# Optimization experiments

Hardware: AMD Instinct MI355X
Metric: run time of the kernel (lower is better)

Reference implementation:

```python
import jax, jax.numpy as jnp
import numpy as np

B, T, DIN, DC, CS = 8, 4096, 1024, 256, 8192
EPS = 1e-12

def _l2norm(x):
    # F.normalize: x / max(||x||_2, eps) along last axis
    n = jnp.sqrt(jnp.sum(x * x, axis=-1, keepdims=True))
    return x / jnp.maximum(n, EPS)

def _wn(v, g):
    # torch weight_norm(dim=0): w = g * v / ||v|| per output row
    n = jnp.sqrt(jnp.sum(v * v, axis=1, keepdims=True))
    return g * v / jnp.maximum(n, EPS)

def setup_inputs() -> dict:
    key = jax.random.key(0)
    k = jax.random.split(key, 4)
    return {
        "z": jax.random.normal(k[0], (B, DIN, T), jnp.float32),
        "in_v": jax.random.normal(k[1], (DC, DIN), jnp.float32) * 0.02,
        "in_g": jnp.ones((DC, 1), jnp.float32),
        "in_b": jnp.zeros((DC,), jnp.float32),
        "out_v": jax.random.normal(k[2], (DIN, DC), jnp.float32) * 0.02,
        "out_g": jnp.ones((DIN, 1), jnp.float32),
        "out_b": jnp.zeros((DIN,), jnp.float32),
        "codebook": jax.random.normal(k[3], (CS, DC), jnp.float32),
    }

def reference(z, in_v, in_g, in_b, out_v, out_g, out_b, codebook):
    b, _, t = z.shape
    w_in = _wn(in_v, in_g)                      # (DC, DIN)
    z_e = jnp.einsum('bdt,cd->bct', z, w_in) + in_b[None, :, None]  # (B, DC, T)

    # decode_latents (eval mode: dropout p=0)
    enc = _l2norm(z_e.transpose(0, 2, 1).reshape(b * t, -1))   # (BT, DC)
    cb = _l2norm(codebook)                                     # (CS, DC)
    dist = (jnp.sum(enc * enc, axis=1, keepdims=True)
            - 2.0 * enc @ cb.T
            + jnp.sum(cb * cb, axis=1)[None, :])               # (BT, CS)
    indices = jnp.argmax(-dist, axis=1).reshape(b, t)          # (B, T)
    z_q = codebook[indices].transpose(0, 2, 1)                 # (B, DC, T)

    commitment_loss = jnp.mean((z_e - jax.lax.stop_gradient(z_q)) ** 2, axis=(1, 2))
    codebook_loss = jnp.mean((z_q - jax.lax.stop_gradient(z_e)) ** 2, axis=(1, 2))

    z_q_st = z_e + jax.lax.stop_gradient(z_q - z_e)            # straight-through
    w_out = _wn(out_v, out_g)                                  # (DIN, DC)
    z_q_out = jnp.einsum('bct,dc->bdt', z_q_st, w_out) + out_b[None, :, None]
    return (z_q_out, commitment_loss, codebook_loss, indices)
```

## Files before the change

### kernel.cpp

```cpp
#include <hip/hip_runtime.h>
#include <stdint.h>

#define BB 8
#define TT 4096
#define DIN 1024
#define DC 256
#define CS 8192
#define EPSF 1e-12f

typedef unsigned short ushort_t;
typedef __attribute__((ext_vector_type(8))) short short8;
typedef __attribute__((ext_vector_type(4))) float f32x4;

constexpr size_t OFF_WIN   = 0;
constexpr size_t OFF_WOUTT = OFF_WIN   + 1048576;
constexpr size_t OFF_CBN   = OFF_WOUTT + 1048576;
constexpr size_t OFF_NRM2  = OFF_CBN   + 8388608;
constexpr size_t OFF_ZE    = OFF_NRM2  + 32768;
constexpr size_t OFF_INV   = OFF_ZE    + 33554432;
constexpr size_t OFF_ENC2  = OFF_INV   + 131072;
constexpr size_t OFF_KEYS  = OFF_ENC2  + 131072;
constexpr size_t OFF_LOSS  = OFF_KEYS  + 262144;
constexpr size_t OFF_WSPL  = OFF_LOSS  + 256;
constexpr size_t OFF_W2T   = OFF_WSPL  + 1048576;
constexpr size_t REQ_WS_ZE = OFF_W2T + 134217728ull;

__device__ __forceinline__ float block_reduce_sum_256(float v, float* sbuf) {
  #pragma unroll
  for (int o = 32; o > 0; o >>= 1) v += __shfl_down(v, o, 64);
  int lane = threadIdx.x & 63, w = threadIdx.x >> 6;
  if (lane == 0) sbuf[w] = v;
  __syncthreads();
  float r = sbuf[0] + sbuf[1] + sbuf[2] + sbuf[3];
  __syncthreads();
  return r;
}

__device__ __forceinline__ ushort_t bf16_rne(float x) {
  unsigned u = __float_as_uint(x);
  unsigned r = (u + 0x7FFFu + ((u >> 16) & 1u)) >> 16;
  return (ushort_t)r;
}
__device__ __forceinline__ float bf16f(ushort_t h) {
  return __uint_as_float(((unsigned)h) << 16);
}

__device__ __forceinline__ int swz4(int r) {
  return (r + (r >> 2)) & 3;
}

__device__ __forceinline__ void async_copy16(const ushort_t* g, ushort_t* lds) {
  __builtin_amdgcn_global_load_lds(
      (const __attribute__((address_space(1))) void*)g,
      (__attribute__((address_space(3))) void*)lds, 16, 0, 0);
}

__device__ __forceinline__ void stage_tile8(const ushort_t* __restrict__ s0,
                                            ushort_t* __restrict__ dstbuf,
                                            const int (&go)[8]) {
  #pragma unroll
  for (int i = 0; i < 8; i++) async_copy16(s0 + go[i], dstbuf + i*512);
}

__device__ __forceinline__ void stage2(const ushort_t* __restrict__ srcbase,
                                       ushort_t* __restrict__ comp,
                                       const int (&go)[2], int wu) {
  async_copy16(srcbase + go[0], comp + wu);
  async_copy16(srcbase + go[1], comp + wu + 4096);
}

#define LD8(base, off) (*(const short8*)((const char*)(base) + (off)))

template<int MH, int CLO>
__device__ __forceinline__ void qmfma(f32x4 (&acc)[8][4],
    const short8 (&fah)[4], const short8 (&fal)[4],
    const short8 (&fbh)[4], const short8 (&fbl)[4]) {
  #pragma unroll
  for (int r = 0; r < 4; r++) {
    #pragma unroll
    for (int c2 = 0; c2 < 2; c2++) {
      f32x4 t = acc[MH*4 + r][CLO + c2];
      t = __builtin_amdgcn_mfma_f32_16x16x32_bf16(fah[r], fbh[CLO + c2], t, 0, 0, 0);
      t = __builtin_amdgcn_mfma_f32_16x16x32_bf16(fal[r], fbh[CLO + c2], t, 0, 0, 0);
      t = __builtin_amdgcn_mfma_f32_16x16x32_bf16(fah[r], fbl[CLO + c2], t, 0, 0, 0);
      acc[MH*4 + r][CLO + c2] = t;
    }
  }
}

__global__ void k_prep_win(const float* __restrict__ v, const float* __restrict__ g,
                           float* __restrict__ w, ushort_t* __restrict__ wh,
                           ushort_t* __restrict__ wl) {
  __shared__ float sb[4];
  int r = blockIdx.x, t = threadIdx.x;
  float xv[4]; float s = 0.f;
  #pragma unroll
  for (int i = 0; i < 4; i++) { xv[i] = v[r*DIN + t + i*256]; s += xv[i]*xv[i]; }
  s = block_reduce_sum_256(s, sb);
  float sc = g[r] / fmaxf(sqrtf(s), EPSF);
  #pragma unroll
  for (int i = 0; i < 4; i++) {
    float val = xv[i] * sc;
    int idx = r*DIN + t + i*256;
    w[idx] = val;
    ushort_t h = bf16_rne(val);
    wh[idx] = h;
    wl[idx] = bf16_rne(val - bf16f(h));
  }
}

__global__ void k_prep_wout(const float* __restrict__ v, const float* __restrict__ g,
                            float* __restrict__ wT) {
  __shared__ float sb[4];
  int r = blockIdx.x, t = threadIdx.x;
  float x = v[r*DC + t];
  float s = block_reduce_sum_256(x*x, sb);
  float sc = g[r] / fmaxf(sqrtf(s), EPSF);
  wT[t*DIN + r] = x * sc;
}

__global__ void k_prep_cb(const float* __restrict__ cb, ushort_t* __restrict__ cbh,
                          ushort_t* __restrict__ cbl, float* __restrict__ nrm2,
                          float* __restrict__ nmraw, float* __restrict__ n2raw) {
  __shared__ float sb[4];
  int j = blockIdx.x, t = threadIdx.x;
  float x = cb[j*DC + t];
  float s = block_reduce_sum_256(x*x, sb);
  float nm = fmaxf(sqrtf(s), EPSF);
  float cn = x / nm;
  ushort_t h = bf16_rne(cn);
  cbh[j*DC + t] = h;
  cbl[j*DC + t] = bf16_rne(cn - bf16f(h));
  float q = block_reduce_sum_256(cn*cn, sb);
  if (t == 0) { nrm2[j] = q; nmraw[j] = nm; n2raw[j] = s; }
}

__global__ void k_split_cbraw(const float* __restrict__ cb, ushort_t* __restrict__ ch,
                              ushort_t* __restrict__ cl) {
  int j = blockIdx.x, t = threadIdx.x;
  float x = cb[j*DC + t];
  ushort_t h = bf16_rne(x);
  ch[j*DC + t] = h;
  cl[j*DC + t] = bf16_rne(x - bf16f(h));
}

__global__ void k_split_wout(const float* __restrict__ v, const float* __restrict__ g,
                             ushort_t* __restrict__ wh, ushort_t* __restrict__ wl) {
  __shared__ float sb[4];
  int r = blockIdx.x, t = threadIdx.x;
  float x = v[r*DC + t];
  float s = block_reduce_sum_256(x*x, sb);
  float sc = g[r] / fmaxf(sqrtf(s), EPSF);
  float val = x * sc;
  ushort_t h = bf16_rne(val);
  wh[r*DC + t] = h;
  wl[r*DC + t] = bf16_rne(val - bf16f(h));
}

template<bool BIAS>
__global__ __launch_bounds__(256) void k_gemm(
    const float* __restrict__ A, const float* __restrict__ Bmat,
    const float* __restrict__ bias, float* __restrict__ C,
    int K, int lda, int ldb, int ldc, size_t strideB, size_t strideC)
{
  __shared__ float As[16][132];
  __shared__ float Bs[16][132];
  const int bn = blockIdx.x * 128;
  const int bm = blockIdx.y * 128;
  const float* Bb = Bmat + (size_t)blockIdx.z * strideB;
  float* Cb = C + (size_t)blockIdx.z * strideC;
  const int tid = threadIdx.x;
  const int tx = tid & 15, ty = tid >> 4;
  const int am = tid & 127, akq = (tid >> 7) * 8;
  const int bk = tid >> 5, bj = (tid & 31) * 4;

  float acc[8][8];
  #pragma unroll
  for (int i = 0; i < 8; i++)
    #pragma unroll
    for (int j = 0; j < 8; j++) acc[i][j] = 0.f;

  for (int k0 = 0; k0 < K; k0 += 16) {
    float4 a0 = *(const float4*)&A[(size_t)(bm+am)*lda + k0 + akq];
    float4 a1 = *(const float4*)&A[(size_t)(bm+am)*lda + k0 + akq + 4];
    float4 b0 = *(const float4*)&Bb[(size_t)(k0+bk)*ldb + bn + bj];
    float4 b1 = *(const float4*)&Bb[(size_t)(k0+bk+8)*ldb + bn + bj];
    As[akq+0][am] = a0.x; As[akq+1][am] = a0.y; As[akq+2][am] = a0.z; As[akq+3][am] = a0.w;
    As[akq+4][am] = a1.x; As[akq+5][am] = a1.y; As[akq+6][am] = a1.z; As[akq+7][am] = a1.w;
    *(float4*)&Bs[bk][bj] = b0;
    *(float4*)&Bs[bk+8][bj] = b1;
    __syncthreads();
    #pragma unroll
    for (int k = 0; k < 16; k++) {
      float av[8], bv[8];
      float4 x0 = *(const float4*)&As[k][tx*4];
      float4 x1 = *(const float4*)&As[k][tx*4+64];
      float4 y0 = *(const float4*)&Bs[k][ty*4];
      float4 y1 = *(const float4*)&Bs[k][ty*4+64];
      av[0]=x0.x; av[1]=x0.y; av[2]=x0.z; av[3]=x0.w;
      av[4]=x1.x; av[5]=x1.y; av[6]=x1.z; av[7]=x1.w;
      bv[0]=y0.x; bv[1]=y0.y; bv[2]=y0.z; bv[3]=y0.w;
      bv[4]=y1.x; bv[5]=y1.y; bv[6]=y1.z; bv[7]=y1.w;
      #pragma unroll
      for (int i = 0; i < 8; i++)
        #pragma unroll
        for (int j = 0; j < 8; j++)
          acc[i][j] += av[i] * bv[j];
    }
    __syncthreads();
  }

  #pragma unroll
  for (int i = 0; i < 8; i++) {
    int mm = bm + ((i < 4) ? tx*4 + i : 64 + tx*4 + (i-4));
    float bia = BIAS ? bias[mm] : 0.f;
    float4 v0 = make_float4(acc[i][0]+bia, acc[i][1]+bia, acc[i][2]+bia, acc[i][3]+bia);
    float4 v1 = make_float4(acc[i][4]+bia, acc[i][5]+bia, acc[i][6]+bia, acc[i][7]+bia);
    *(float4*)&Cb[(size_t)mm*ldc + bn + ty*4]      = v0;
    *(float4*)&Cb[(size_t)mm*ldc + bn + 64 + ty*4] = v1;
  }
}

__global__ void k_split_z(const float* __restrict__ z, ushort_t* __restrict__ zhi,
                          ushort_t* __restrict__ zlo) {
  __shared__ float tile[64][65];
  int b = blockIdx.z, t0 = blockIdx.x * 64, d0 = blockIdx.y * 64;
  int tx = threadIdx.x & 63, ty = threadIdx.x >> 6;
  const float* zb = z + (size_t)b*DIN*TT;
  #pragma unroll
  for (int i = 0; i < 16; i++) {
    int d = i*4 + ty;
    tile[d][tx] = zb[(size_t)(d0+d)*TT + t0 + tx];
  }
  __syncthreads();
  #pragma unroll
  for (int i = 0; i < 16; i++) {
    int t = i*4 + ty;
    float val = tile[tx][t];
    ushort_t h = bf16_rne(val);
    size_t o = ((size_t)(b*TT + t0 + t))*DIN + d0 + tx;
    zhi[o] = h;
    zlo[o] = bf16_rne(val - bf16f(h));
  }
}

__global__ __launch_bounds__(512) void k_ze_enc(
    const ushort_t* __restrict__ zth, const ushort_t* __restrict__ ztl,
    const ushort_t* __restrict__ wh, const ushort_t* __restrict__ wl,
    const float* __restrict__ in_b,
    ushort_t* __restrict__ ehi, ushort_t* __restrict__ elo,
    float* __restrict__ inv, float* __restrict__ enc2, float* __restrict__ e2raw)
{
  __shared__ ushort_t smem[49152];
  __shared__ float e2s[128][4];
  __shared__ float sIv[128];

  ushort_t* sAh = smem;
  ushort_t* sAl = smem + 8192;
  ushort_t* sBh = smem + 16384;
  ushort_t* sBl = smem + 32768;

  const int t0 = blockIdx.x * 128;
  const int b  = blockIdx.y;
  const int tid = threadIdx.x;
  const int lane = tid & 63;
  const int wave = tid >> 6;
  const int wr = wave >> 2, wc = wave & 3;
  const int ml = lane & 15, quad = lane >> 4;
  const size_t r0 = (size_t)b*TT + t0;

  const ushort_t* gAh = zth + r0*DIN;
  const ushort_t* gAl = ztl + r0*DIN;

  int goA;
  { int r = tid >> 2, c = tid & 3; int g = c ^ swz4(r); goA = r*DIN + (g << 3); }
  int goB[2];
  #pragma unroll
  for (int l = 0; l < 2; l++) {
    int chunk = l*512 + tid;
    int r = chunk >> 2, c = chunk & 3;
    int g = c ^ swz4(r);
    goB[l] = r*DIN + (g << 3);
  }
  const int wu = wave * 512;

  int offA[4], offB[4];
  #pragma unroll
  for (int i = 0; i < 4; i++) {
    int r = wr*64 + i*16 + ml;
    int p = quad ^ swz4(r);
    offA[i] = r*64 + p*16;
  }
  #pragma unroll
  for (int i = 0; i < 4; i++) {
    int r = wc*64 + i*16 + ml;
    int p = quad ^ swz4(r);
    offB[i] = r*64 + p*16;
  }

  f32x4 acc[4][4];
  #pragma unroll
  for (int i = 0; i < 4; i++)
    #pragma unroll
    for (int j = 0; j < 4; j++) acc[i][j] = (f32x4)0.f;

  async_copy16(gAh + goA, sAh + wu);
  async_copy16(gAl + goA, sAl + wu);
  stage2(wh, sBh, goB, wu);
  stage2(wl, sBl, goB, wu);

  for (int it = 0; it < 32; ++it) {
    __syncthreads();
    if (it < 31) {
      const int nb = (it+1) & 1;
      async_copy16(gAh + goA + (it+1)*32, sAh + nb*4096 + wu);
      async_copy16(gAl + goA + (it+1)*32, sAl + nb*4096 + wu);
      stage2(wh + (it+1)*32, sBh + nb*8192, goB, wu);
      stage2(wl + (it+1)*32, sBl + nb*8192, goB, wu);
    }
    const char* pAh = (const char*)(sAh + (it & 1)*4096);
    const char* pAl = (const char*)(sAl + (it & 1)*4096);
    const char* pBh = (const char*)(sBh + (it & 1)*8192);
    const char* pBl = (const char*)(sBl + (it & 1)*8192);

    short8 fbh[4], fbl[4];
    #pragma unroll
    for (int ci = 0; ci < 4; ci++) {
      fbh[ci] = LD8(pBh, offB[ci]);
      fbl[ci] = LD8(pBl, offB[ci]);
    }
    #pragma unroll
    for (int ri = 0; ri < 4; ri++) {
      short8 ah = LD8(pAh, offA[ri]);
      short8 al = LD8(pAl, offA[ri]);
      #pragma unroll
      for (int ci = 0; ci < 4; ci++) {
        acc[ri][ci] = __builtin_amdgcn_mfma_f32_16x16x32_bf16(ah, fbh[ci], acc[ri][ci], 0, 0, 0);
        acc[ri][ci] = __builtin_amdgcn_mfma_f32_16x16x32_bf16(al, fbh[ci], acc[ri][ci], 0, 0, 0);
        acc[ri][ci] = __builtin_amdgcn_mfma_f32_16x16x32_bf16(ah, fbl[ci], acc[ri][ci], 0, 0, 0);
      }
    }
  }

  float bia[4];
  #pragma unroll
  for (int ci = 0; ci < 4; ci++) bia[ci] = in_b[wc*64 + ci*16 + ml];

  #pragma unroll
  for (int ri = 0; ri < 4; ri++) {
    #pragma unroll
    for (int reg = 0; reg < 4; reg++) {
      float p = 0.f;
      #pragma unroll
      for (int ci = 0; ci < 4; ci++) {
        float v = acc[ri][ci][reg] + bia[ci];
        acc[ri][ci][reg] = v;
        p += v*v;
      }
      #pragma unroll
      for (int off = 1; off < 16; off <<= 1) p += __shfl_xor(p, off);
      if (ml == 0) e2s[wr*64 + ri*16 + quad*4 + reg][wc] = p;
    }
  }
  __syncthreads();
  if (tid < 128) {
    float s = ((e2s[tid][0] + e2s[tid][1]) + e2s[tid][2]) + e2s[tid][3];
    float iv = 1.f / fmaxf(sqrtf(s), EPSF);
    sIv[tid] = iv;
    inv[r0 + tid]   = iv;
    enc2[r0 + tid]  = (s * iv) * iv;
    e2raw[r0 + tid] = s;
  }
  __syncthreads();

  ushort_t* tb = smem;
  #pragma unroll
  for (int ri = 0; ri < 4; ri++) {
    #pragma unroll
    for (int reg = 0; reg < 4; reg++) {
      int t_loc = wr*64 + ri*16 + quad*4 + reg;
      float ivt = sIv[t_loc];
      #pragma unroll
      for (int ci = 0; ci < 4; ci++) {
        int c_loc = wc*64 + ci*16 + ml;
        tb[t_loc*256 + c_loc] = bf16_rne(acc[ri][ci][reg] * ivt);
      }
    }
  }
  __syncthreads();
  #pragma unroll
  for (int p = 0; p < 8; p++) {
    int ch = p*512 + tid;
    *(short8*)(ehi + r0*DC + (size_t)ch*8) = *(const short8*)(tb + ch*8);
  }
  __syncthreads();
  #pragma unroll
  for (int ri = 0; ri < 4; ri++) {
    #pragma unroll
    for (int reg = 0; reg < 4; reg++) {
      int t_loc = wr*64 + ri*16 + quad*4 + reg;
      float ivt = sIv[t_loc];
      #pragma unroll
      for (int ci = 0; ci < 4; ci++) {
        int c_loc = wc*64 + ci*16 + ml;
        float v = acc[ri][ci][reg] * ivt;
        ushort_t h = bf16_rne(v);
        tb[t_loc*256 + c_loc] = bf16_rne(v - bf16f(h));
      }
    }
  }
  __syncthreads();
  #pragma unroll
  for (int p = 0; p < 8; p++) {
    int ch = p*512 + tid;
    *(short8*)(elo + r0*DC + (size_t)ch*8) = *(const short8*)(tb + ch*8);
  }
}

__global__ __launch_bounds__(256) void k_w2t_mfma(
    const ushort_t* __restrict__ ah_g, const ushort_t* __restrict__ al_g,
    const ushort_t* __restrict__ bh_g, const ushort_t* __restrict__ bl_g,
    float* __restrict__ C)
{
  __shared__ ushort_t As_hi[2][4096];
  __shared__ ushort_t As_lo[2][4096];
  __shared__ ushort_t Bs_hi[2][4096];
  __shared__ ushort_t Bs_lo[2][4096];

  const int m0 = blockIdx.x * 128;
  const int n0 = blockIdx.y * 128;
  const int tid = threadIdx.x;
  const int lane = tid & 63;
  const int wave = tid >> 6;
  const int wr = wave >> 1, wc = wave & 1;
  const int m = lane & 15, quad = lane >> 4;

  const ushort_t* src; ushort_t* dst;
  {
    size_t aoff = (size_t)m0 * DC;
    size_t boff = (size_t)n0 * DC;
    if      (wave == 0) { src = ah_g + aoff; dst = &As_hi[0][0]; }
    else if (wave == 1) { src = al_g + aoff; dst = &As_lo[0][0]; }
    else if (wave == 2) { src = bh_g + boff; dst = &Bs_hi[0][0]; }
    else                { src = bl_g + boff; dst = &Bs_lo[0][0]; }
  }
  const int rr = lane >> 2, cc = lane & 3;

  int goT[8];
  #pragma unroll
  for (int i = 0; i < 8; i++) {
    int r = i*16 + rr;
    int g = cc ^ swz4(r);
    goT[i] = r*DC + (g << 3);
  }

  int offA[4], offB[4];
  #pragma unroll
  for (int ri = 0; ri < 4; ri++) {
    int r = wr*64 + ri*16 + m;
    int p = quad ^ swz4(r);
    offA[ri] = r*64 + p*16;
  }
  #pragma unroll
  for (int ci = 0; ci < 4; ci++) {
    int r = wc*64 + ci*16 + m;
    int p = quad ^ swz4(r);
    offB[ci] = r*64 + p*16;
  }

  f32x4 acc[4][4];
  #pragma unroll
  for (int i = 0; i < 4; i++)
    #pragma unroll
    for (int j = 0; j < 4; j++) acc[i][j] = (f32x4)0.f;

  stage_tile8(src, dst, goT);

  for (int it = 0; it < 8; ++it) {
    __syncthreads();
    if (it < 7) stage_tile8(src + (it+1)*32, dst + ((it+1)&1)*4096, goT);
    const int bo = (it & 1) << 13;

    short8 bh[4], bl[4];
    #pragma unroll
    for (int ci = 0; ci < 4; ci++) {
      bh[ci] = *(const short8*)((const char*)Bs_hi + bo + offB[ci]);
      bl[ci] = *(const short8*)((const char*)Bs_lo + bo + offB[ci]);
    }
    #pragma unroll
    for (int ri = 0; ri < 4; ri++) {
      short8 ah = *(const short8*)((const char*)As_hi + bo + offA[ri]);
      short8 al = *(const short8*)((const char*)As_lo + bo + offA[ri]);
      #pragma unroll
      for (int ci = 0; ci < 4; ci++) {
        acc[ri][ci] = __builtin_amdgcn_mfma_f32_16x16x32_bf16(ah, bh[ci], acc[ri][ci], 0, 0, 0);
        acc[ri][ci] = __builtin_amdgcn_mfma_f32_16x16x32_bf16(al, bh[ci], acc[ri][ci], 0, 0, 0);
        acc[ri][ci] = __builtin_amdgcn_mfma_f32_16x16x32_bf16(ah, bl[ci], acc[ri][ci], 0, 0, 0);
      }
    }
  }

  #pragma unroll
  for (int ri = 0; ri < 4; ri++) {
    int m_loc = wr*64 + ri*16 + quad*4;
    #pragma unroll
    for (int ci = 0; ci < 4; ci++) {
      int n_loc = wc*64 + ci*16 + m;
      #pragma unroll
      for (int reg = 0; reg < 4; reg++) {
        C[(size_t)(m0 + m_loc + reg)*DIN + n0 + n_loc] = acc[ri][ci][reg];
      }
    }
  }
}

__global__ void k_colnorm(const float* __restrict__ ze, float* __restrict__ inv,
                          float* __restrict__ enc2) {
  int r = blockIdx.x * 128 + threadIdx.x;
  int b = r >> 12, t = r & 4095;
  const float* p = ze + (size_t)b*DC*TT + t;
  float s = 0.f;
  for (int c = 0; c < DC; c++) { float x = p[(size_t)c*TT]; s += x*x; }
  float iv = 1.f / fmaxf(sqrtf(s), EPSF);
  inv[r] = iv;
  enc2[r] = (s * iv) * iv;
}

__global__ void k_split_enc(const float* __restrict__ ze, const float* __restrict__ inv,
                            ushort_t* __restrict__ ehi, ushort_t* __restrict__ elo) {
  __shared__ float tile[64][65];
  int b = blockIdx.z, t0 = blockIdx.x * 64, c0 = blockIdx.y * 64;
  int tx = threadIdx.x & 63, ty = threadIdx.x >> 6;
  const float* zb = ze + (size_t)b*DC*TT;
  #pragma unroll
  for (int i = 0; i < 16; i++) {
    int c = i*4 + ty;
    tile[c][tx] = zb[(size_t)(c0+c)*TT + t0 + tx];
  }
  __syncthreads();
  #pragma unroll
  for (int i = 0; i < 16; i++) {
    int t = i*4 + ty;
    float iv = inv[b*TT + t0 + t];
    float val = tile[tx][t] * iv;
    ushort_t h = bf16_rne(val);
    size_t o = ((size_t)(b*TT + t0 + t))*DC + c0 + tx;
    ehi[o] = h;
    elo[o] = bf16_rne(val - bf16f(h));
  }
}

__global__ void k_lossidx(const float* __restrict__ ze, const float* __restrict__ cb,
                          const unsigned long long* __restrict__ keys,
                          float* __restrict__ loss_sums, float* __restrict__ out_idx)
{
  __shared__ float sb[4];
  __shared__ int sj[64];
  int b = blockIdx.y, t0 = blockIdx.x * 64;
  int tid = threadIdx.x;
  if (tid < 64) {
    unsigned long long k = keys[(size_t)b*TT + t0 + tid];
    int j = (int)(unsigned)(k & 0xFFFFFFFFull);
    sj[tid] = j;
    out_idx[(size_t)b*TT + t0 + tid] = (float)j;
  }
  __syncthreads();
  int tt = tid & 63, tc = tid >> 6;
  const float* zb = ze + (size_t)b*DC*TT + t0;
  int j = sj[tt];
  float s = 0.f;
  for (int ci = 0; ci < 64; ci++) {
    int c = tc + ci*4;
    float zev = zb[(size_t)c*TT + tt];
    float zqv = cb[(size_t)j*DC + c];
    float d = zev - zqv;
    s += d*d;
  }
  s = block_reduce_sum_256(s, sb);
  if (tid == 0) atomicAdd(&loss_sums[b], s);
}

__global__ __launch_bounds__(512, 2) void k_dist_mfma(
    const ushort_t* __restrict__ ehi, const ushort_t* __restrict__ elo,
    const ushort_t* __restrict__ cbh, const ushort_t* __restrict__ cbl,
    const float* __restrict__ nrm2, const float* __restrict__ enc2,
    unsigned long long* __restrict__ keys)
{
  __shared__ ushort_t sAh[2][8192];
  __shared__ ushort_t sAl[2][8192];
  __shared__ ushort_t sBh[2][8192];
  __shared__ ushort_t sBl[2][8192];
  __shared__ float sE2[256], sN2[256];
  __shared__ unsigned long long rkey[256];

  const int j0 = blockIdx.x * 256;
  const size_t r0 = (size_t)blockIdx.y * 256;
  const int tid = threadIdx.x;
  const int lane = tid & 63;
  const int wave = tid >> 6;
  const int wr = wave >> 2, wc = wave & 3;
  const int ml = lane & 15, quad = lane >> 4;

  if (tid < 256) {
    sE2[tid] = enc2[r0 + tid];
    sN2[tid] = nrm2[j0 + tid];
    rkey[tid] = 0xFFFFFFFFFFFFFFFFull;
  }

  const ushort_t* gAh = ehi + r0 * DC;
  const ushort_t* gAl = elo + r0 * DC;
  const ushort_t* gBh = cbh + (size_t)j0 * DC;
  const ushort_t* gBl = cbl + (size_t)j0 * DC;

  int goS[2];
  #pragma unroll
  for (int l = 0; l < 2; l++) {
    int chunk = l*512 + tid;
    int r = chunk >> 2, c = chunk & 3;
    int g = c ^ swz4(r);
    goS[l] = r*DC + (g << 3);
  }
  const int wu = wave * 512;

  int offA[8], offB[4];
  #pragma unroll
  for (int i = 0; i < 8; i++) {
    int r = wr*128 + i*16 + ml;
    int p = quad ^ swz4(r);
    offA[i] = r*64 + p*16;
  }
  #pragma unroll
  for (int i = 0; i < 4; i++) {
    int r = wc*64 + i*16 + ml;
    int p = quad ^ swz4(r);
    offB[i] = r*64 + p*16;
  }

  f32x4 acc[8][4];
  #pragma unroll
  for (int i = 0; i < 8; i++)
    #pragma unroll
    for (int j = 0; j < 4; j++) acc[i][j] = (f32x4)0.f;

  stage2(gBh,      &sBh[0][0], goS, wu);
  stage2(gBl,      &sBl[0][0], goS, wu);
  stage2(gAh,      &sAh[0][0], goS, wu);
  stage2(gAl,      &sAl[0][0], goS, wu);
  stage2(gBh + 32, &sBh[1][0], goS, wu);
  stage2(gBl + 32, &sBl[1][0], goS, wu);
  asm volatile("s_waitcnt vmcnt(4)" ::: "memory");
  asm volatile("s_waitcnt lgkmcnt(0)" ::: "memory");
  __builtin_amdgcn_s_barrier();
  __builtin_amdgcn_sched_barrier(0);

  short8 fa_h[4], fa_l[4], fb_h[4], fb_l[4];

  #pragma unroll 2
  for (int k = 0; k < 8; k++) {
    const int cb = k & 1, nb = cb ^ 1;
    const char* pAh = (const char*)&sAh[cb][0];
    const char* pAl = (const char*)&sAl[cb][0];
    const char* pBh = (const char*)&sBh[cb][0];
    const char* pBl = (const char*)&sBl[cb][0];
    __builtin_amdgcn_sched_barrier(0);

    #pragma unroll
    for (int i = 0; i < 4; i++) { fa_h[i] = LD8(pAh, offA[i]); fa_l[i] = LD8(pAl, offA[i]); }
    #pragma unroll
    for (int i = 0; i < 2; i++) { fb_h[i] = LD8(pBh, offB[i]); fb_l[i] = LD8(pBl, offB[i]); }
    if (k < 7) stage2(gAh + (size_t)(k+1)*32, &sAh[nb][0], goS, wu);
    __builtin_amdgcn_s_barrier();
    __builtin_amdgcn_s_setprio(1);
    qmfma<0, 0>(acc, fa_h, fa_l, fb_h, fb_l);
    __builtin_amdgcn_s_setprio(0);
    __builtin_amdgcn_s_barrier();

    #pragma unroll
    for (int i = 2; i < 4; i++) { fb_h[i] = LD8(pBh, offB[i]); fb_l[i] = LD8(pBl, offB[i]); }
    if (k < 7) stage2(gAl + (size_t)(k+1)*32, &sAl[nb][0], goS, wu);
    __builtin_amdgcn_s_barrier();
    __builtin_amdgcn_s_setprio(1);
    qmfma<0, 2>(acc, fa_h, fa_l, fb_h, fb_l);
    __builtin_amdgcn_s_setprio(0);
    __builtin_amdgcn_s_barrier();

    #pragma unroll
    for (int i = 0; i < 4; i++) { fa_h[i] = LD8(pAh, offA[4+i]); fa_l[i] = LD8(pAl, offA[4+i]); }
    if (k < 6) {
      stage2(gBh + (size_t)(k+2)*32, &sBh[cb][0], goS, wu);
      stage2(gBl + (size_t)(k+2)*32, &sBl[cb][0], goS, wu);
    }
    __builtin_amdgcn_s_barrier();
    __builtin_amdgcn_s_setprio(1);
    qmfma<1, 2>(acc, fa_h, fa_l, fb_h, fb_l);
    qmfma<1, 0>(acc, fa_h, fa_l, fb_h, fb_l);
    __builtin_amdgcn_s_setprio(0);
    if (k < 6) { asm volatile("s_waitcnt vmcnt(4)" ::: "memory"); }
    else       { asm volatile("s_waitcnt vmcnt(0)" ::: "memory"); }
    __builtin_amdgcn_s_barrier();
  }

  #pragma unroll
  for (int ri = 0; ri < 8; ri++) {
    #pragma unroll
    for (int reg = 0; reg < 4; reg++) {
      int t_loc = wr*128 + ri*16 + quad*4 + reg;
      float e2 = sE2[t_loc];
      unsigned long long best = 0xFFFFFFFFFFFFFFFFull;
      #pragma unroll
      for (int ci = 0; ci < 4; ci++) {
        int j_loc = wc*64 + ci*16 + ml;
        float d = e2 - 2.0f * acc[ri][ci][reg];
        d = d + sN2[j_loc];
        unsigned long long key =
            ((unsigned long long)__float_as_uint(d) << 32) | (unsigned)(j0 + j_loc);
        best = key < best ? key : best;
      }
      #pragma unroll
      for (int off = 1; off < 16; off <<= 1) {
        unsigned long long o = __shfl_xor(best, off);
        best = o < best ? o : best;
      }
      if (ml == 0) atomicMin(&rkey[t_loc], best);
    }
  }
  __syncthreads();
  if (tid < 256) atomicMin(&keys[r0 + tid], rkey[tid]);
}

__global__ void k_lossrec(const unsigned long long* __restrict__ keys,
                          const float* __restrict__ enc2, const float* __restrict__ nrm2,
                          const float* __restrict__ e2raw, const float* __restrict__ inv,
                          const float* __restrict__ nmraw, const float* __restrict__ n2raw,
                          float* __restrict__ loss_sums, float* __restrict__ out_idx)
{
  __shared__ float sb[4];
  int r = blockIdx.x * 256 + threadIdx.x;
  int b = r >> 12;
  unsigned long long k = keys[r];
  int j = (int)(unsigned)(k & 0xFFFFFFFFull);
  float d = __uint_as_float((unsigned)(k >> 32));
  out_idx[r] = (float)j;
  float dotn = 0.5f * (enc2[r] + nrm2[j] - d);
  float dot_raw = nmraw[j] * dotn / inv[r];
  float le = e2raw[r] - 2.f*dot_raw + n2raw[j];
  float s = block_reduce_sum_256(le, sb);
  if (threadIdx.x == 0) atomicAdd(&loss_sums[b], s);
}

__global__ void k_losswrite(const float* __restrict__ loss_sums, float* __restrict__ out_loss) {
  int i = threadIdx.x;
  if (i < 8) {
    float v = loss_sums[i] * (1.f/1048576.f);
    out_loss[i] = v;
    out_loss[8 + i] = v;
  }
}

__global__ void k_outgather(const float* __restrict__ W2T,
                            const unsigned long long* __restrict__ keys,
                            const float* __restrict__ out_b, float* __restrict__ out)
{
  __shared__ float tile[64][65];
  __shared__ int sj[64];
  int b = blockIdx.y, t0 = blockIdx.x * 64;
  int tid = threadIdx.x;
  if (tid < 64) sj[tid] = (int)(unsigned)(keys[(size_t)b*TT + t0 + tid] & 0xFFFFFFFFull);
  __syncthreads();
  float* ob = out + (size_t)b*DIN*TT;
  int dd = tid & 63, tq = tid >> 6;
  for (int d0 = 0; d0 < DIN; d0 += 64) {
    #pragma unroll
    for (int i = 0; i < 16; i++) {
      int t = tq*16 + i;
      tile[t][dd] = W2T[(size_t)sj[t]*DIN + d0 + dd];
    }
    __syncthreads();
    #pragma unroll
    for (int i = 0; i < 16; i++) {
      int d = tq*16 + i;
      ob[(size_t)(d0+d)*TT + t0 + dd] = tile[dd][d] + out_b[d0+d];
    }
    __syncthreads();
  }
}

extern "C" void kernel_launch(void* const* d_in, const int* in_sizes, int n_in,
                              void* d_out, int out_size, void* d_ws, size_t ws_size,
                              hipStream_t stream) {
  const float* z        = (const float*)d_in[0];
  const float* in_v     = (const float*)d_in[1];
  const float* in_g     = (const float*)d_in[2];
  const float* in_b     = (const float*)d_in[3];
  const float* out_v    = (const float*)d_in[4];
  const float* out_g    = (const float*)d_in[5];
  const float* out_b    = (const float*)d_in[6];
  const float* codebook = (const float*)d_in[7];

  char* w = (char*)d_ws;
  float* w_in   = (float*)(w + OFF_WIN);
  float* w_outT = (float*)(w + OFF_WOUTT);
  float* e2raw  = (float*)(w + OFF_WOUTT);
  float* nmraw  = (float*)(w + OFF_WOUTT + 131072);
  float* n2raw  = (float*)(w + OFF_WOUTT + 163840);
  ushort_t* cb_hi = (ushort_t*)(w + OFF_CBN);
  ushort_t* cb_lo = cb_hi + (size_t)CS*DC;
  float* nrm2   = (float*)(w + OFF_NRM2);
  float* z_e    = (float*)(w + OFF_ZE);
  ushort_t* enc_hi_m = (ushort_t*)(w + OFF_ZE);
  ushort_t* enc_lo_m = enc_hi_m + (size_t)BB*TT*DC;
  float* inv    = (float*)(w + OFF_INV);
  float* enc2   = (float*)(w + OFF_ENC2);
  unsigned long long* keys = (unsigned long long*)(w + OFF_KEYS);
  float* loss_sums = (float*)(w + OFF_LOSS);
  ushort_t* w_hi = (ushort_t*)(w + OFF_WSPL);
  ushort_t* w_lo = w_hi + (size_t)DC*DIN;
  ushort_t* zt_hi = (ushort_t*)(w + OFF_W2T);
  ushort_t* zt_lo = zt_hi + (size_t)BB*TT*DIN;
  ushort_t* enc_hi_fb = (ushort_t*)(w + OFF_W2T);
  ushort_t* enc_lo_fb = enc_hi_fb + (size_t)BB*TT*DC;
  float* W2T    = (float*)(w + OFF_W2T);
  ushort_t* cbr_hi  = (ushort_t*)(w + OFF_W2T + 33554432);
  ushort_t* cbr_lo  = cbr_hi + (size_t)CS*DC;
  ushort_t* wout_hi = (ushort_t*)(w + OFF_W2T + 33554432 + 8388608);
  ushort_t* wout_lo = wout_hi + (size_t)DIN*DC;

  float* out      = (float*)d_out;
  float* out_loss = out + (size_t)BB*DIN*TT;
  float* out_idx  = out_loss + 16;

  hipMemsetAsync(keys, 0xFF, 32768ull*8, stream);
  hipMemsetAsync(loss_sums, 0, 32, stream);

  const bool mfma_path = (ws_size >= REQ_WS_ZE);

  k_prep_win <<<256, 256, 0, stream>>>(in_v, in_g, w_in, w_hi, w_lo);
  k_prep_cb  <<<8192, 256, 0, stream>>>(codebook, cb_hi, cb_lo, nrm2, nmraw, n2raw);

  if (mfma_path) {
    k_split_z<<<dim3(64, 16, 8), 256, 0, stream>>>(z, zt_hi, zt_lo);
    k_ze_enc<<<dim3(32, 8), 512, 0, stream>>>(
        zt_hi, zt_lo, w_hi, w_lo, in_b, enc_hi_m, enc_lo_m, inv, enc2, e2raw);

    k_dist_mfma<<<dim3(32, 128), 512, 0, stream>>>(
        enc_hi_m, enc_lo_m, cb_hi, cb_lo, nrm2, enc2, keys);

    k_lossrec<<<128, 256, 0, stream>>>(
        keys, enc2, nrm2, e2raw, inv, nmraw, n2raw, loss_sums, out_idx);
    k_losswrite<<<1, 64, 0, stream>>>(loss_sums, out_loss);

    k_split_cbraw<<<8192, 256, 0, stream>>>(codebook, cbr_hi, cbr_lo);
    k_split_wout <<<1024, 256, 0, stream>>>(out_v, out_g, wout_hi, wout_lo);
    k_w2t_mfma<<<dim3(64, 8), 256, 0, stream>>>(cbr_hi, cbr_lo, wout_hi, wout_lo, W2T);
  } else {
    k_prep_wout<<<1024, 256, 0, stream>>>(out_v, out_g, w_outT);
    k_gemm<true><<<dim3(32, 2, 8), 256, 0, stream>>>(
        w_in, z, in_b, z_e, 1024, 1024, 4096, 4096,
        (size_t)DIN*TT, (size_t)DC*TT);
    k_colnorm<<<256, 128, 0, stream>>>(z_e, inv, enc2);
    k_split_enc<<<dim3(64, 4, 8), 256, 0, stream>>>(z_e, inv, enc_hi_fb, enc_lo_fb);

    k_dist_mfma<<<dim3(32, 128), 512, 0, stream>>>(
        enc_hi_fb, enc_lo_fb, cb_hi, cb_lo, nrm2, enc2, keys);

    k_lossidx<<<dim3(64, 8), 256, 0, stream>>>(z_e, codebook, keys, loss_sums, out_idx);
    k_losswrite<<<1, 64, 0, stream>>>(loss_sums, out_loss);

    k_gemm<false><<<dim3(8, 64, 1), 256, 0, stream>>>(
        codebook, w_outT, nullptr, W2T, 256, 256, 1024, 1024,
        (size_t)0, (size_t)0);
  }

  k_outgather<<<dim3(64, 8), 256, 0, stream>>>(W2T, keys, out_b, out);
}
```

Before: 877.8 us.

## Fuse z bf16 split and transpose into z_e GEMM load path; merge codebook splits

Removes the separate k_split_z pass, which wrote bf16 hi/lo transposed copies of z to global memory. The GEMM now loads fp32 z directly, splits it into hi/lo in registers and writes swizzled shared-memory tiles, with the register prefetch overlapping the MFMA loop. The raw-codebook hi/lo split is also folded into k_prep_cb, and k_split_wout moves earlier in the launch order. This saves a large global write-and-reread and a few launches, at the cost of synchronous global loads and scalar shared-memory stores replacing the async copies inside the GEMM.

```diff
diff --git a/kernel.cpp b/kernel.cpp
--- a/kernel.cpp
+++ b/kernel.cpp
@@ -121,10 +121,14 @@
 
 __global__ void k_prep_cb(const float* __restrict__ cb, ushort_t* __restrict__ cbh,
                           ushort_t* __restrict__ cbl, float* __restrict__ nrm2,
-                          float* __restrict__ nmraw, float* __restrict__ n2raw) {
+                          float* __restrict__ nmraw, float* __restrict__ n2raw,
+                          ushort_t* __restrict__ crh, ushort_t* __restrict__ crl) {
   __shared__ float sb[4];
   int j = blockIdx.x, t = threadIdx.x;
   float x = cb[j*DC + t];
+  ushort_t hr = bf16_rne(x);
+  crh[j*DC + t] = hr;
+  crl[j*DC + t] = bf16_rne(x - bf16f(hr));
   float s = block_reduce_sum_256(x*x, sb);
   float nm = fmaxf(sqrtf(s), EPSF);
   float cn = x / nm;
@@ -133,15 +137,6 @@
   cbl[j*DC + t] = bf16_rne(cn - bf16f(h));
   float q = block_reduce_sum_256(cn*cn, sb);
   if (t == 0) { nrm2[j] = q; nmraw[j] = nm; n2raw[j] = s; }
-}
-
-__global__ void k_split_cbraw(const float* __restrict__ cb, ushort_t* __restrict__ ch,
-                              ushort_t* __restrict__ cl) {
-  int j = blockIdx.x, t = threadIdx.x;
-  float x = cb[j*DC + t];
-  ushort_t h = bf16_rne(x);
-  ch[j*DC + t] = h;
-  cl[j*DC + t] = bf16_rne(x - bf16f(h));
 }
 
 __global__ void k_split_wout(const float* __restrict__ v, const float* __restrict__ g,
@@ -221,31 +216,8 @@
   }
 }
 
-__global__ void k_split_z(const float* __restrict__ z, ushort_t* __restrict__ zhi,
-                          ushort_t* __restrict__ zlo) {
-  __shared__ float tile[64][65];
-  int b = blockIdx.z, t0 = blockIdx.x * 64, d0 = blockIdx.y * 64;
-  int tx = threadIdx.x & 63, ty = threadIdx.x >> 6;
-  const float* zb = z + (size_t)b*DIN*TT;
-  #pragma unroll
-  for (int i = 0; i < 16; i++) {
-    int d = i*4 + ty;
-    tile[d][tx] = zb[(size_t)(d0+d)*TT + t0 + tx];
-  }
-  __syncthreads();
-  #pragma unroll
-  for (int i = 0; i < 16; i++) {
-    int t = i*4 + ty;
-    float val = tile[tx][t];
-    ushort_t h = bf16_rne(val);
-    size_t o = ((size_t)(b*TT + t0 + t))*DIN + d0 + tx;
-    zhi[o] = h;
-    zlo[o] = bf16_rne(val - bf16f(h));
-  }
-}
-
 __global__ __launch_bounds__(512) void k_ze_enc(
-    const ushort_t* __restrict__ zth, const ushort_t* __restrict__ ztl,
+    const float* __restrict__ z,
     const ushort_t* __restrict__ wh, const ushort_t* __restrict__ wl,
     const float* __restrict__ in_b,
     ushort_t* __restrict__ ehi, ushort_t* __restrict__ elo,
@@ -269,11 +241,15 @@
   const int ml = lane & 15, quad = lane >> 4;
   const size_t r0 = (size_t)b*TT + t0;
 
-  const ushort_t* gAh = zth + r0*DIN;
-  const ushort_t* gAl = ztl + r0*DIN;
-
-  int goA;
-  { int r = tid >> 2, c = tid & 3; int g = c ^ swz4(r); goA = r*DIN + (g << 3); }
+  const int dl = tid >> 4, tg = tid & 15;
+  const float* zsrc = z + (size_t)b*DIN*TT + (size_t)dl*TT + t0 + tg*8;
+  int idxA[8];
+  #pragma unroll
+  for (int i = 0; i < 8; i++) {
+    int t = tg*8 + i;
+    idxA[i] = t*32 + (((dl >> 3) ^ swz4(t)) << 3) + (dl & 7);
+  }
+
   int goB[2];
   #pragma unroll
   for (int l = 0; l < 2; l++) {
@@ -304,24 +280,33 @@
     #pragma unroll
     for (int j = 0; j < 4; j++) acc[i][j] = (f32x4)0.f;
 
-  async_copy16(gAh + goA, sAh + wu);
-  async_copy16(gAl + goA, sAl + wu);
+  float4 va = *(const float4*)(zsrc);
+  float4 vb = *(const float4*)(zsrc + 4);
   stage2(wh, sBh, goB, wu);
   stage2(wl, sBl, goB, wu);
+  {
+    float vv[8] = {va.x, va.y, va.z, va.w, vb.x, vb.y, vb.z, vb.w};
+    #pragma unroll
+    for (int i = 0; i < 8; i++) {
+      ushort_t h = bf16_rne(vv[i]);
+      sAh[idxA[i]] = h;
+      sAl[idxA[i]] = bf16_rne(vv[i] - bf16f(h));
+    }
+  }
 
   for (int it = 0; it < 32; ++it) {
     __syncthreads();
+    const int cbuf = it & 1, nb = cbuf ^ 1;
     if (it < 31) {
-      const int nb = (it+1) & 1;
-      async_copy16(gAh + goA + (it+1)*32, sAh + nb*4096 + wu);
-      async_copy16(gAl + goA + (it+1)*32, sAl + nb*4096 + wu);
+      va = *(const float4*)(zsrc + (size_t)(it+1)*32*TT);
+      vb = *(const float4*)(zsrc + (size_t)(it+1)*32*TT + 4);
       stage2(wh + (it+1)*32, sBh + nb*8192, goB, wu);
       stage2(wl + (it+1)*32, sBl + nb*8192, goB, wu);
     }
-    const char* pAh = (const char*)(sAh + (it & 1)*4096);
-    const char* pAl = (const char*)(sAl + (it & 1)*4096);
-    const char* pBh = (const char*)(sBh + (it & 1)*8192);
-    const char* pBl = (const char*)(sBl + (it & 1)*8192);
+    const char* pAh = (const char*)(sAh + cbuf*4096);
+    const char* pAl = (const char*)(sAl + cbuf*4096);
+    const char* pBh = (const char*)(sBh + cbuf*8192);
+    const char* pBl = (const char*)(sBl + cbuf*8192);
 
     short8 fbh[4], fbl[4];
     #pragma unroll
@@ -338,6 +323,18 @@
         acc[ri][ci] = __builtin_amdgcn_mfma_f32_16x16x32_bf16(ah, fbh[ci], acc[ri][ci], 0, 0, 0);
         acc[ri][ci] = __builtin_amdgcn_mfma_f32_16x16x32_bf16(al, fbh[ci], acc[ri][ci], 0, 0, 0);
         acc[ri][ci] = __builtin_amdgcn_mfma_f32_16x16x32_bf16(ah, fbl[ci], acc[ri][ci], 0, 0, 0);
+      }
+    }
+
+    if (it < 31) {
+      ushort_t* dAh = sAh + nb*4096;
+      ushort_t* dAl = sAl + nb*4096;
+      float vv[8] = {va.x, va.y, va.z, va.w, vb.x, vb.y, vb.z, vb.w};
+      #pragma unroll
+      for (int i = 0; i < 8; i++) {
+        ushort_t h = bf16_rne(vv[i]);
+        dAh[idxA[i]] = h;
+        dAl[idxA[i]] = bf16_rne(vv[i] - bf16f(h));
       }
     }
   }
@@ -815,8 +812,6 @@
   float* loss_sums = (float*)(w + OFF_LOSS);
   ushort_t* w_hi = (ushort_t*)(w + OFF_WSPL);
   ushort_t* w_lo = w_hi + (size_t)DC*DIN;
-  ushort_t* zt_hi = (ushort_t*)(w + OFF_W2T);
-  ushort_t* zt_lo = zt_hi + (size_t)BB*TT*DIN;
   ushort_t* enc_hi_fb = (ushort_t*)(w + OFF_W2T);
   ushort_t* enc_lo_fb = enc_hi_fb + (size_t)BB*TT*DC;
   float* W2T    = (float*)(w + OFF_W2T);
@@ -835,12 +830,14 @@
   const bool mfma_path = (ws_size >= REQ_WS_ZE);
 
   k_prep_win <<<256, 256, 0, stream>>>(in_v, in_g, w_in, w_hi, w_lo);
-  k_prep_cb  <<<8192, 256, 0, stream>>>(codebook, cb_hi, cb_lo, nrm2, nmraw, n2raw);
+  k_prep_cb  <<<8192, 256, 0, stream>>>(codebook, cb_hi, cb_lo, nrm2, nmraw, n2raw,
+                                        cbr_hi, cbr_lo);
 
   if (mfma_path) {
-    k_split_z<<<dim3(64, 16, 8), 256, 0, stream>>>(z, zt_hi, zt_lo);
+    k_split_wout<<<1024, 256, 0, stream>>>(out_v, out_g, wout_hi, wout_lo);
+
     k_ze_enc<<<dim3(32, 8), 512, 0, stream>>>(
-        zt_hi, zt_lo, w_hi, w_lo, in_b, enc_hi_m, enc_lo_m, inv, enc2, e2raw);
+        z, w_hi, w_lo, in_b, enc_hi_m, enc_lo_m, inv, enc2, e2raw);
 
     k_dist_mfma<<<dim3(32, 128), 512, 0, stream>>>(
         enc_hi_m, enc_lo_m, cb_hi, cb_lo, nrm2, enc2, keys);
@@ -849,8 +846,6 @@
         keys, enc2, nrm2, e2raw, inv, nmraw, n2raw, loss_sums, out_idx);
     k_losswrite<<<1, 64, 0, stream>>>(loss_sums, out_loss);
 
-    k_split_cbraw<<<8192, 256, 0, stream>>>(codebook, cbr_hi, cbr_lo);
-    k_split_wout <<<1024, 256, 0, stream>>>(out_v, out_g, wout_hi, wout_lo);
     k_w2t_mfma<<<dim3(64, 8), 256, 0, stream>>>(cbr_hi, cbr_lo, wout_hi, wout_lo, W2T);
   } else {
     k_prep_wout<<<1024, 256, 0, stream>>>(out_v, out_g, w_outT);
```

Measured after the change: 830.8 us. -5.4%, faster.
